# Kernel tuning notes

Measured on AMD Instinct MI355X. Metric: run time of the kernel, lower is better.

The kernel has to match this reference:

```python
import jax, jax.numpy as jnp
import numpy as np

# Model dims
B, S, H, E, I, K = 2, 2048, 1024, 8, 1024, 2
ALPHA, LIMIT = 1.702, 7.0  # gpt_oss activation constants (module defaults)


def setup_inputs() -> dict:
    key = jax.random.key(0)
    ks = jax.random.split(key, 5)
    sc = 0.02
    return {
        "hidden_states": jax.random.normal(ks[0], (B, S, H), jnp.float32),
        "router_weight": jax.random.normal(ks[1], (H, E), jnp.float32) * sc,
        "gate_up_proj": jax.random.normal(ks[2], (E, H, 2 * I), jnp.float32) * sc,
        "gate_up_proj_bias": jnp.zeros((E, 2 * I), jnp.float32),
        "down_proj": jax.random.normal(ks[3], (E, I, H), jnp.float32) * sc,
        "down_proj_bias": jnp.zeros((E, H), jnp.float32),
    }


def reference(hidden_states, router_weight, gate_up_proj, gate_up_proj_bias,
              down_proj, down_proj_bias):
    Bt, St, Ht = hidden_states.shape
    x = hidden_states.reshape(-1, Ht)           # [T, H], T = B*S
    T = x.shape[0]

    # Router: linear -> top-k -> softmax over selected logits (gpt_oss style)
    logits = x @ router_weight                  # [T, E]
    top_vals, top_idx = jax.lax.top_k(logits, K)
    scores = jax.nn.softmax(top_vals, axis=-1)  # [T, K]
    # Sparse combine weights: w[t, e] = score if e selected for t, else 0
    w = jnp.zeros((T, E), x.dtype).at[jnp.arange(T)[:, None], top_idx].set(scores)

    # Fused gate+up projection for every expert (dense equivalent of grouped GEMM;
    # unselected experts get zero combine weight so math matches sparse path)
    gu = jnp.einsum('th,ehf->tef', x, gate_up_proj) + gate_up_proj_bias  # [T, E, 2I]
    gate = gu[..., ::2]                         # interleaved gate (default)
    up = gu[..., 1::2]
    gate = jnp.minimum(gate, LIMIT)
    up = jnp.clip(up, -LIMIT, LIMIT)
    glu = gate * jax.nn.sigmoid(gate * ALPHA)
    act = (up + 1.0) * glu                      # [T, E, I]

    down = jnp.einsum('tei,eih->teh', act, down_proj) + down_proj_bias  # [T, E, H]

    # Weighted combine over experts (all-to-all combine is identity at D=1)
    out = jnp.einsum('te,teh->th', w, down)     # [T, H]
    return out.reshape(Bt, St, Ht)
```

## Files before the change

kernel.cpp:

```cpp
#include <hip/hip_runtime.h>
#include <hip/hip_bf16.h>
#include <cstdint>
#include <cstddef>

constexpr int T_TOK = 4096;
constexpr int H_DIM = 1024;
constexpr int E_NUM = 8;
constexpr int I_DIM = 1024;
constexpr int F2    = 2048;
constexpr float ALPHA = 1.702f;
constexpr float LIMIT = 7.0f;
constexpr int BM = 256;
constexpr int BK = 32;
constexpr int NT = 32;
constexpr int MAXT = 40;

using u16    = unsigned short;
using bf16x8 = __attribute__((ext_vector_type(8))) __bf16;
using s16x8  = __attribute__((ext_vector_type(8))) short;
using f32x4  = __attribute__((ext_vector_type(4))) float;

constexpr size_t WS_W1T  = 0;
constexpr size_t WS_DOWN = 0;
constexpr size_t WS_W2T  = 33554432;
constexpr size_t WS_ACT  = 50331648;
constexpr size_t WS_ETOK = 71303168;
constexpr size_t WS_POS  = 71434240;
constexpr size_t WS_CNT  = 71467008;
constexpr size_t WS_ROWB = 71467040;
constexpr size_t WS_ASGN = 71467072;
constexpr size_t WS_TOPE = 71468096;
constexpr size_t WS_TOPW = 71484480;
constexpr size_t WS_XBF  = 71517248;
constexpr size_t WS_NEED = 79905856;

__device__ __forceinline__ u16 f2bf(float f) {
    union { float f; unsigned u; } v; v.f = f;
    return (u16)((v.u + 0x7FFFu + ((v.u >> 16) & 1u)) >> 16);
}
__device__ __forceinline__ float bf2f(u16 u) {
    union { unsigned u; float f; } v; v.u = (unsigned)u << 16; return v.f;
}

__device__ __forceinline__ s16x8 pack8(float4 a, float4 b) {
    s16x8 r;
    r[0] = (short)f2bf(a.x); r[1] = (short)f2bf(a.y);
    r[2] = (short)f2bf(a.z); r[3] = (short)f2bf(a.w);
    r[4] = (short)f2bf(b.x); r[5] = (short)f2bf(b.y);
    r[6] = (short)f2bf(b.z); r[7] = (short)f2bf(b.w);
    return r;
}

__device__ __forceinline__ void gload16(const void* g, void* l) {
    __builtin_amdgcn_global_load_lds((const __attribute__((address_space(1))) unsigned*)g,
                                     (__attribute__((address_space(3))) unsigned*)l,
                                     16, 0, 0);
}

__device__ __forceinline__ void pipe_sync() {
    __builtin_amdgcn_sched_barrier(0);
    asm volatile("s_waitcnt vmcnt(0) lgkmcnt(0)" ::: "memory");
    __builtin_amdgcn_s_barrier();
    __builtin_amdgcn_sched_barrier(0);
}

__global__ __launch_bounds__(256) void k_xbf(const float* __restrict__ x,
                                             u16* __restrict__ xbf) {
    const size_t i = ((size_t)blockIdx.x * 256 + threadIdx.x) * 8;
    float4 a = *(const float4*)(x + i);
    float4 b = *(const float4*)(x + i + 4);
    *(s16x8*)(xbf + i) = pack8(a, b);
}

__global__ __launch_bounds__(256) void k_transpose_w1(const float* __restrict__ in,
                                                      u16* __restrict__ out) {
    __shared__ float tile[64][65];
    const int e = blockIdx.z, c0 = blockIdx.x * 64, h0 = blockIdx.y * 64;
    const int tid = threadIdx.x;
    const float* src = in + ((size_t)e * H_DIM + h0) * F2 + c0;
#pragma unroll
    for (int i = 0; i < 4; ++i) {
        int r = (tid >> 4) + i * 16, c = (tid & 15) * 4;
        float4 v = *(const float4*)(src + (size_t)r * F2 + c);
        tile[r][c] = v.x; tile[r][c + 1] = v.y; tile[r][c + 2] = v.z; tile[r][c + 3] = v.w;
    }
    __syncthreads();
    const int c = tid >> 2, hseg = (tid & 3) * 16;
    const int g = c & 1;
    const int f = (c0 + c) >> 1;
    s16x8 o0, o1;
#pragma unroll
    for (int j = 0; j < 8; ++j) o0[j] = (short)f2bf(tile[hseg + j][c]);
#pragma unroll
    for (int j = 0; j < 8; ++j) o1[j] = (short)f2bf(tile[hseg + 8 + j][c]);
    const int pan = f >> 6;
    const int brow = g * 64 + (f & 63);
    const int h1 = h0 + hseg;
    const int kt = h1 >> 5;
    const int s0 = (h1 & 31) >> 3;
    const int xr = (brow >> 1) & 3;
    u16* blk = out + (((size_t)(e * 16 + pan) * 32 + kt) << 12);
    *(s16x8*)(blk + brow * 32 + ((s0 ^ xr) << 3))       = o0;
    *(s16x8*)(blk + brow * 32 + (((s0 + 1) ^ xr) << 3)) = o1;
}

__global__ __launch_bounds__(256) void k_transpose_w2(const float* __restrict__ in,
                                                      u16* __restrict__ out) {
    __shared__ float tile[64][65];
    const int e = blockIdx.z, h0 = blockIdx.x * 64, i0 = blockIdx.y * 64;
    const int tid = threadIdx.x;
    const float* src = in + ((size_t)e * I_DIM + i0) * H_DIM + h0;
#pragma unroll
    for (int i = 0; i < 4; ++i) {
        int r = (tid >> 4) + i * 16, c = (tid & 15) * 4;
        float4 v = *(const float4*)(src + (size_t)r * H_DIM + c);
        tile[r][c] = v.x; tile[r][c + 1] = v.y; tile[r][c + 2] = v.z; tile[r][c + 3] = v.w;
    }
    __syncthreads();
    const int c = tid >> 2, iseg = (tid & 3) * 16;
    s16x8 o0, o1;
#pragma unroll
    for (int j = 0; j < 8; ++j) o0[j] = (short)f2bf(tile[iseg + j][c]);
#pragma unroll
    for (int j = 0; j < 8; ++j) o1[j] = (short)f2bf(tile[iseg + 8 + j][c]);
    const int hcol = h0 + c;
    const int pan = hcol >> 7;
    const int brow = hcol & 127;
    const int i1 = i0 + iseg;
    const int kt = i1 >> 5;
    const int s0 = (i1 & 31) >> 3;
    const int xr = (brow >> 1) & 3;
    u16* blk = out + (((size_t)(e * 8 + pan) * 32 + kt) << 12);
    *(s16x8*)(blk + brow * 32 + ((s0 ^ xr) << 3))       = o0;
    *(s16x8*)(blk + brow * 32 + (((s0 + 1) ^ xr) << 3)) = o1;
}

__global__ __launch_bounds__(256) void k_router_top2(const float* __restrict__ x,
                                                     const float* __restrict__ rw,
                                                     int* __restrict__ tope,
                                                     float2* __restrict__ topw) {
    const int wave = threadIdx.x >> 6, lane = threadIdx.x & 63;
    const int t = blockIdx.x * 4 + wave;
    const float* xr = x + (size_t)t * H_DIM;
    float acc[E_NUM];
#pragma unroll
    for (int e = 0; e < E_NUM; ++e) acc[e] = 0.f;
    for (int h = lane; h < H_DIM; h += 64) {
        float xv = xr[h];
        const float* r = rw + h * E_NUM;
#pragma unroll
        for (int e = 0; e < E_NUM; ++e) acc[e] += xv * r[e];
    }
#pragma unroll
    for (int e = 0; e < E_NUM; ++e) {
        float v = acc[e];
#pragma unroll
        for (int o = 32; o > 0; o >>= 1) v += __shfl_down(v, o);
        acc[e] = v;
    }
    if (lane == 0) {
        int e0 = 0; float v0 = acc[0];
#pragma unroll
        for (int e = 1; e < E_NUM; ++e) if (acc[e] > v0) { v0 = acc[e]; e0 = e; }
        int e1 = -1; float v1 = -3.4e38f;
#pragma unroll
        for (int e = 0; e < E_NUM; ++e) if (e != e0 && acc[e] > v1) { v1 = acc[e]; e1 = e; }
        float ew = expf(v1 - v0);
        float inv = 1.f / (1.f + ew);
        tope[t] = e0 | (e1 << 8);
        topw[t] = make_float2(inv, ew * inv);
    }
}

__global__ __launch_bounds__(256) void k_router_scatter(const int* __restrict__ tope,
                                                        int* __restrict__ cnt,
                                                        int* __restrict__ ent_tok,
                                                        int2* __restrict__ pos) {
    __shared__ int lcnt[E_NUM];
    __shared__ int gbase[E_NUM];
    const int tid = threadIdx.x;
    const int t = blockIdx.x * 256 + tid;
    if (tid < E_NUM) lcnt[tid] = 0;
    __syncthreads();
    const int pk = tope[t];
    const int e0 = pk & 0xff, e1 = pk >> 8;
    const int o0 = atomicAdd(&lcnt[e0], 1);
    const int o1 = atomicAdd(&lcnt[e1], 1);
    __syncthreads();
    if (tid < E_NUM) gbase[tid] = atomicAdd(&cnt[tid], lcnt[tid]);
    __syncthreads();
    const int p0 = gbase[e0] + o0;
    const int p1 = gbase[e1] + o1;
    ent_tok[e0 * T_TOK + p0] = t;
    ent_tok[e1 * T_TOK + p1] = t;
    pos[t] = make_int2(p0, p1);
}

__global__ void k_schedule(const int* __restrict__ cnt, int* __restrict__ rowbase,
                           int* __restrict__ assign) {
    if (threadIdx.x == 0) {
        int rb = 0, na = 0;
        for (int e = 0; e < E_NUM; ++e) {
            rowbase[e] = rb;
            int nt = (cnt[e] + BM - 1) >> 8;
            for (int m = 0; m < nt; ++m) assign[na++] = (e << 16) | m;
            rb += cnt[e];
            rb = (rb + 255) & ~255;
        }
        for (; na < MAXT; ++na) assign[na] = -1;
    }
}

__global__ __launch_bounds__(512, 4) void k_gemm1(
    const u16* __restrict__ xbf, const u16* __restrict__ w1t,
    const float* __restrict__ bias, const int* __restrict__ ent_tok,
    const int* __restrict__ cnt, const int* __restrict__ rowbase,
    const int* __restrict__ assign, u16* __restrict__ act) {
    const int a = assign[blockIdx.y];
    if (a < 0) return;
    const int e = a >> 16, mt = a & 0xffff;
    const int pan = blockIdx.x;
    const int j0 = pan * 64;
    const int cs = cnt[e], r0 = mt * BM;
    __shared__ __align__(16) u16 As[2][BM * BK];
    __shared__ __align__(16) u16 Bs[2][128 * BK];
    const int tid = threadIdx.x, lane = tid & 63, wv = tid >> 6;
    const int lr = lane >> 2;
    const int sm = (lane & 3) ^ ((lr >> 1) & 3);
    const u16* asrc[2]; int dofsA[2];
#pragma unroll
    for (int j = 0; j < 2; ++j) {
        const int row = wv * 32 + j * 16 + lr;
        const int aent = r0 + row;
        const int tok = (aent < cs) ? ent_tok[e * T_TOK + aent] : 0;
        asrc[j] = xbf + (size_t)tok * H_DIM + sm * 8;
        dofsA[j] = (wv * 32 + j * 16) * BK;
    }
    const u16* bblk = w1t + ((size_t)(e * 16 + pan) * 32) * 4096 + wv * 512 + lane * 8;
    const int dofsB = wv * 512;
    const int wm = wv >> 1, wn = wv & 1;
    const int lcol = lane & 15, lk = lane >> 4;
    int aoff[4], goff[2], uoff[2];
#pragma unroll
    for (int mi = 0; mi < 4; ++mi) {
        const int r = wm * 64 + mi * 16 + lcol;
        aoff[mi] = r * 64 + ((lk ^ ((r >> 1) & 3)) << 4);
    }
#pragma unroll
    for (int nj = 0; nj < 2; ++nj) {
        const int rg_ = wn * 32 + nj * 16 + lcol;
        const int ru  = 64 + rg_;
        goff[nj] = rg_ * 64 + ((lk ^ ((rg_ >> 1) & 3)) << 4);
        uoff[nj] = ru  * 64 + ((lk ^ ((ru  >> 1) & 3)) << 4);
    }
    f32x4 ag[4][2], au[4][2];
    const f32x4 z = {0.f, 0.f, 0.f, 0.f};
#pragma unroll
    for (int mi = 0; mi < 4; ++mi) { ag[mi][0] = z; ag[mi][1] = z; au[mi][0] = z; au[mi][1] = z; }
#pragma unroll
    for (int j = 0; j < 2; ++j) gload16(asrc[j], &As[0][dofsA[j]]);
    gload16(bblk, &Bs[0][dofsB]);
    pipe_sync();
    int cur = 0;
    for (int t = 0; t < NT; ++t) {
        if (t + 1 < NT) {
            const int kn = (t + 1) * BK;
            u16* Ad = As[cur ^ 1]; u16* Bd = Bs[cur ^ 1];
#pragma unroll
            for (int j = 0; j < 2; ++j) gload16(asrc[j] + kn, Ad + dofsA[j]);
            gload16(bblk + (t + 1) * 4096, Bd + dofsB);
        }
        const char* Ab = (const char*)As[cur];
        const char* Bb = (const char*)Bs[cur];
        bf16x8 af[4];
#pragma unroll
        for (int mi = 0; mi < 4; ++mi) af[mi] = *(const bf16x8*)(Ab + aoff[mi]);
        const bf16x8 g0 = *(const bf16x8*)(Bb + goff[0]);
        const bf16x8 g1 = *(const bf16x8*)(Bb + goff[1]);
        const bf16x8 u0 = *(const bf16x8*)(Bb + uoff[0]);
        const bf16x8 u1 = *(const bf16x8*)(Bb + uoff[1]);
#pragma unroll
        for (int mi = 0; mi < 4; ++mi) {
            ag[mi][0] = __builtin_amdgcn_mfma_f32_16x16x32_bf16(af[mi], g0, ag[mi][0], 0, 0, 0);
            au[mi][0] = __builtin_amdgcn_mfma_f32_16x16x32_bf16(af[mi], u0, au[mi][0], 0, 0, 0);
            ag[mi][1] = __builtin_amdgcn_mfma_f32_16x16x32_bf16(af[mi], g1, ag[mi][1], 0, 0, 0);
            au[mi][1] = __builtin_amdgcn_mfma_f32_16x16x32_bf16(af[mi], u1, au[mi][1], 0, 0, 0);
        }
        pipe_sync();
        cur ^= 1;
    }
    const int rbase = rowbase[e];
#pragma unroll
    for (int mi = 0; mi < 4; ++mi) {
#pragma unroll
        for (int nj = 0; nj < 2; ++nj) {
            const int col = j0 + wn * 32 + nj * 16 + lcol;
            const float bg_ = bias[e * F2 + 2 * col];
            const float bu_ = bias[e * F2 + 2 * col + 1];
            const int kt = col >> 5, slot = (col & 31) >> 3, ke = col & 7;
#pragma unroll
            for (int rg = 0; rg < 4; ++rg) {
                const int r = wm * 64 + mi * 16 + lk * 4 + rg;
                if (r0 + r < cs) {
                    float gv = ag[mi][nj][rg] + bg_;
                    float uv = au[mi][nj][rg] + bu_;
                    gv = fminf(gv, LIMIT);
                    uv = fminf(fmaxf(uv, -LIMIT), LIMIT);
                    const float glu = gv / (1.f + expf(-ALPHA * gv));
                    const int grow = rbase + r0 + r;
                    const int rr = grow & 255;
                    act[((size_t)(grow >> 8) * 32 + kt) * 8192 + rr * 32 +
                        ((slot ^ ((rr >> 1) & 3)) << 3) + ke] = f2bf((uv + 1.f) * glu);
                }
            }
        }
    }
}

__global__ __launch_bounds__(512, 4) void k_gemm2(
    const u16* __restrict__ actb, const u16* __restrict__ w2t,
    const int* __restrict__ cnt, const int* __restrict__ rowbase,
    const int* __restrict__ assign, u16* __restrict__ down) {
    const int a = assign[blockIdx.y];
    if (a < 0) return;
    const int e = a >> 16, mt = a & 0xffff;
    const int pan = blockIdx.x;
    const int n0 = pan * 128;
    const int cs = cnt[e], r0 = mt * BM, rbase = rowbase[e];
    __shared__ __align__(16) u16 As[2][BM * BK];
    __shared__ __align__(16) u16 Bs[2][128 * BK];
    const int tid = threadIdx.x, lane = tid & 63, wv = tid >> 6;
    const u16* ablk = actb + ((size_t)((rbase + r0) >> 8) * 32) * 8192 + wv * 1024 + lane * 8;
    const u16* bblk = w2t + ((size_t)(e * 8 + pan) * 32) * 4096 + wv * 512 + lane * 8;
    const int dofsB = wv * 512;
    const int wm = wv >> 1, wn = wv & 1;
    const int lcol = lane & 15, lk = lane >> 4;
    int aoff[4], boff[4];
#pragma unroll
    for (int mi = 0; mi < 4; ++mi) {
        const int r = wm * 64 + mi * 16 + lcol;
        aoff[mi] = r * 64 + ((lk ^ ((r >> 1) & 3)) << 4);
    }
#pragma unroll
    for (int nj = 0; nj < 4; ++nj) {
        const int b = wn * 64 + nj * 16 + lcol;
        boff[nj] = b * 64 + ((lk ^ ((b >> 1) & 3)) << 4);
    }
    f32x4 acc[4][4];
    const f32x4 z = {0.f, 0.f, 0.f, 0.f};
#pragma unroll
    for (int mi = 0; mi < 4; ++mi)
#pragma unroll
        for (int nj = 0; nj < 4; ++nj) acc[mi][nj] = z;
#pragma unroll
    for (int j = 0; j < 2; ++j) gload16(ablk + j * 512, &As[0][wv * 1024 + j * 512]);
    gload16(bblk, &Bs[0][dofsB]);
    pipe_sync();
    int cur = 0;
    for (int t = 0; t < NT; ++t) {
        if (t + 1 < NT) {
            u16* Ad = As[cur ^ 1]; u16* Bd = Bs[cur ^ 1];
#pragma unroll
            for (int j = 0; j < 2; ++j)
                gload16(ablk + (t + 1) * 8192 + j * 512, Ad + wv * 1024 + j * 512);
            gload16(bblk + (t + 1) * 4096, Bd + dofsB);
        }
        const char* Ab = (const char*)As[cur];
        const char* Bb = (const char*)Bs[cur];
        bf16x8 af[4], bf_[4];
#pragma unroll
        for (int mi = 0; mi < 4; ++mi) af[mi]  = *(const bf16x8*)(Ab + aoff[mi]);
#pragma unroll
        for (int nj = 0; nj < 4; ++nj) bf_[nj] = *(const bf16x8*)(Bb + boff[nj]);
#pragma unroll
        for (int mi = 0; mi < 4; ++mi)
#pragma unroll
            for (int nj = 0; nj < 4; ++nj)
                acc[mi][nj] = __builtin_amdgcn_mfma_f32_16x16x32_bf16(af[mi], bf_[nj], acc[mi][nj], 0, 0, 0);
        pipe_sync();
        cur ^= 1;
    }
#pragma unroll
    for (int mi = 0; mi < 4; ++mi) {
#pragma unroll
        for (int nj = 0; nj < 4; ++nj) {
            const int col = n0 + wn * 64 + nj * 16 + lcol;
#pragma unroll
            for (int rg = 0; rg < 4; ++rg) {
                const int r = wm * 64 + mi * 16 + lk * 4 + rg;
                if (r0 + r < cs)
                    down[(size_t)(rbase + r0 + r) * H_DIM + col] = f2bf(acc[mi][nj][rg]);
            }
        }
    }
}

__global__ __launch_bounds__(256) void k_combine(
    const int* __restrict__ tope, const float2* __restrict__ topw,
    const int2* __restrict__ pos, const int* __restrict__ rowb,
    const float* __restrict__ b2, const u16* __restrict__ down,
    float* __restrict__ out) {
    const int t = blockIdx.x;
    const int c = threadIdx.x * 4;
    const int pk = tope[t];
    const int e0 = pk & 0xff, e1 = pk >> 8;
    const int2 pp = pos[t];
    const float2 w = topw[t];
    const size_t ro0 = (size_t)(rowb[e0] + pp.x) * H_DIM;
    const size_t ro1 = (size_t)(rowb[e1] + pp.y) * H_DIM;
    ushort4 d0 = *(const ushort4*)(down + ro0 + c);
    ushort4 d1 = *(const ushort4*)(down + ro1 + c);
    float4 bb0 = *(const float4*)(b2 + e0 * H_DIM + c);
    float4 bb1 = *(const float4*)(b2 + e1 * H_DIM + c);
    float4 o;
    o.x = w.x * (bf2f(d0.x) + bb0.x) + w.y * (bf2f(d1.x) + bb1.x);
    o.y = w.x * (bf2f(d0.y) + bb0.y) + w.y * (bf2f(d1.y) + bb1.y);
    o.z = w.x * (bf2f(d0.z) + bb0.z) + w.y * (bf2f(d1.z) + bb1.z);
    o.w = w.x * (bf2f(d0.w) + bb0.w) + w.y * (bf2f(d1.w) + bb1.w);
    *(float4*)(out + (size_t)t * H_DIM + c) = o;
}

extern "C" void kernel_launch(void* const* d_in, const int* in_sizes, int n_in,
                              void* d_out, int out_size, void* d_ws, size_t ws_size,
                              hipStream_t stream) {
    const float* x   = (const float*)d_in[0];
    const float* rw  = (const float*)d_in[1];
    const float* w1  = (const float*)d_in[2];
    const float* b1  = (const float*)d_in[3];
    const float* w2  = (const float*)d_in[4];
    const float* b2  = (const float*)d_in[5];
    float* out = (float*)d_out;
    char* ws = (char*)d_ws;

    if (ws_size < WS_NEED) return;

    u16*    W1T  = (u16*)(ws + WS_W1T);
    u16*    DOWN = (u16*)(ws + WS_DOWN);
    u16*    W2T  = (u16*)(ws + WS_W2T);
    u16*    ACT  = (u16*)(ws + WS_ACT);
    int*    ETOK = (int*)(ws + WS_ETOK);
    int2*   POS  = (int2*)(ws + WS_POS);
    int*    CNT  = (int*)(ws + WS_CNT);
    int*    ROWB = (int*)(ws + WS_ROWB);
    int*    ASGN = (int*)(ws + WS_ASGN);
    int*    TOPE = (int*)(ws + WS_TOPE);
    float2* TOPW = (float2*)(ws + WS_TOPW);
    u16*    XBF  = (u16*)(ws + WS_XBF);

    hipMemsetAsync(CNT, 0, E_NUM * sizeof(int), stream);

    k_xbf<<<T_TOK * H_DIM / 2048, 256, 0, stream>>>(x, XBF);
    k_transpose_w1<<<dim3(32, 16, 8), 256, 0, stream>>>(w1, W1T);
    k_transpose_w2<<<dim3(16, 16, 8), 256, 0, stream>>>(w2, W2T);
    k_router_top2<<<T_TOK / 4, 256, 0, stream>>>(x, rw, TOPE, TOPW);
    k_router_scatter<<<T_TOK / 256, 256, 0, stream>>>(TOPE, CNT, ETOK, POS);
    k_schedule<<<1, 64, 0, stream>>>(CNT, ROWB, ASGN);
    k_gemm1<<<dim3(16, MAXT), 512, 0, stream>>>(XBF, W1T, b1, ETOK, CNT, ROWB, ASGN, ACT);
    k_gemm2<<<dim3(8, MAXT), 512, 0, stream>>>(ACT, W2T, CNT, ROWB, ASGN, DOWN);
    k_combine<<<T_TOK, 256, 0, stream>>>(TOPE, TOPW, POS, ROWB, b2, DOWN, out);
}
```

Baseline: 163.4 us.

## Triple-buffer LDS stages in both expert GEMMs with partial vmcnt waits

Both grouped GEMM kernels move from a double-buffered LDS pipeline to a three-stage ring. Each iteration issues the loads two K-steps ahead, and a partial `s_waitcnt vmcnt` waits only for the current stage's data instead of draining every outstanding load. The aim is to hide more global-load latency behind the MFMA work. In exchange, LDS use per block grows by half, which can cut how many blocks fit on a CU.

```diff
diff --git a/kernel.cpp b/kernel.cpp
--- a/kernel.cpp
+++ b/kernel.cpp
@@ -57,12 +57,9 @@
                                      16, 0, 0);
 }
 
-__device__ __forceinline__ void pipe_sync() {
-    __builtin_amdgcn_sched_barrier(0);
-    asm volatile("s_waitcnt vmcnt(0) lgkmcnt(0)" ::: "memory");
-    __builtin_amdgcn_s_barrier();
-    __builtin_amdgcn_sched_barrier(0);
-}
+#define SB0() __builtin_amdgcn_sched_barrier(0)
+#define BARC() do { SB0(); __builtin_amdgcn_s_barrier(); SB0(); } while (0)
+#define WVM(n) do { SB0(); asm volatile("s_waitcnt vmcnt(" #n ")" ::: "memory"); } while (0)
 
 __global__ __launch_bounds__(256) void k_xbf(const float* __restrict__ x,
                                              u16* __restrict__ xbf) {
@@ -222,8 +219,8 @@
     const int pan = blockIdx.x;
     const int j0 = pan * 64;
     const int cs = cnt[e], r0 = mt * BM;
-    __shared__ __align__(16) u16 As[2][BM * BK];
-    __shared__ __align__(16) u16 Bs[2][128 * BK];
+    __shared__ __align__(16) u16 As[3][BM * BK];
+    __shared__ __align__(16) u16 Bs[3][128 * BK];
     const int tid = threadIdx.x, lane = tid & 63, wv = tid >> 6;
     const int lr = lane >> 2;
     const int sm = (lane & 3) ^ ((lr >> 1) & 3);
@@ -257,21 +254,25 @@
     const f32x4 z = {0.f, 0.f, 0.f, 0.f};
 #pragma unroll
     for (int mi = 0; mi < 4; ++mi) { ag[mi][0] = z; ag[mi][1] = z; au[mi][0] = z; au[mi][1] = z; }
-#pragma unroll
-    for (int j = 0; j < 2; ++j) gload16(asrc[j], &As[0][dofsA[j]]);
-    gload16(bblk, &Bs[0][dofsB]);
-    pipe_sync();
-    int cur = 0;
+
+#define G1_STAGE(kt, Ad, Bd) do {                                           \
+        const int kn_ = (kt) * BK;                                          \
+        _Pragma("unroll") for (int j = 0; j < 2; ++j)                       \
+            gload16(asrc[j] + kn_, (Ad) + dofsA[j]);                        \
+        gload16(bblk + (size_t)(kt) * 4096, (Bd) + dofsB);                  \
+    } while (0)
+
+    G1_STAGE(0, As[0], Bs[0]);
+    G1_STAGE(1, As[1], Bs[1]);
+    u16 *Ar = As[0], *An = As[1], *Af = As[2];
+    u16 *Br = Bs[0], *Bn = Bs[1], *Bf = Bs[2];
     for (int t = 0; t < NT; ++t) {
-        if (t + 1 < NT) {
-            const int kn = (t + 1) * BK;
-            u16* Ad = As[cur ^ 1]; u16* Bd = Bs[cur ^ 1];
-#pragma unroll
-            for (int j = 0; j < 2; ++j) gload16(asrc[j] + kn, Ad + dofsA[j]);
-            gload16(bblk + (t + 1) * 4096, Bd + dofsB);
-        }
-        const char* Ab = (const char*)As[cur];
-        const char* Bb = (const char*)Bs[cur];
+        if (t + 2 < NT) { G1_STAGE(t + 2, Af, Bf); WVM(6); }
+        else if (t + 1 < NT) { WVM(3); }
+        else { WVM(0); }
+        BARC();
+        const char* Ab = (const char*)Ar;
+        const char* Bb = (const char*)Br;
         bf16x8 af[4];
 #pragma unroll
         for (int mi = 0; mi < 4; ++mi) af[mi] = *(const bf16x8*)(Ab + aoff[mi]);
@@ -286,9 +287,11 @@
             ag[mi][1] = __builtin_amdgcn_mfma_f32_16x16x32_bf16(af[mi], g1, ag[mi][1], 0, 0, 0);
             au[mi][1] = __builtin_amdgcn_mfma_f32_16x16x32_bf16(af[mi], u1, au[mi][1], 0, 0, 0);
         }
-        pipe_sync();
-        cur ^= 1;
-    }
+        BARC();
+        u16* tA = Ar; Ar = An; An = Af; Af = tA;
+        u16* tB = Br; Br = Bn; Bn = Bf; Bf = tB;
+    }
+#undef G1_STAGE
     const int rbase = rowbase[e];
 #pragma unroll
     for (int mi = 0; mi < 4; ++mi) {
@@ -327,8 +330,8 @@
     const int pan = blockIdx.x;
     const int n0 = pan * 128;
     const int cs = cnt[e], r0 = mt * BM, rbase = rowbase[e];
-    __shared__ __align__(16) u16 As[2][BM * BK];
-    __shared__ __align__(16) u16 Bs[2][128 * BK];
+    __shared__ __align__(16) u16 As[3][BM * BK];
+    __shared__ __align__(16) u16 Bs[3][128 * BK];
     const int tid = threadIdx.x, lane = tid & 63, wv = tid >> 6;
     const u16* ablk = actb + ((size_t)((rbase + r0) >> 8) * 32) * 8192 + wv * 1024 + lane * 8;
     const u16* bblk = w2t + ((size_t)(e * 8 + pan) * 32) * 4096 + wv * 512 + lane * 8;
@@ -352,21 +355,25 @@
     for (int mi = 0; mi < 4; ++mi)
 #pragma unroll
         for (int nj = 0; nj < 4; ++nj) acc[mi][nj] = z;
-#pragma unroll
-    for (int j = 0; j < 2; ++j) gload16(ablk + j * 512, &As[0][wv * 1024 + j * 512]);
-    gload16(bblk, &Bs[0][dofsB]);
-    pipe_sync();
-    int cur = 0;
+
+#define G2_STAGE(kt, Ad, Bd) do {                                           \
+        _Pragma("unroll") for (int j = 0; j < 2; ++j)                       \
+            gload16(ablk + (size_t)(kt) * 8192 + j * 512,                   \
+                    (Ad) + wv * 1024 + j * 512);                            \
+        gload16(bblk + (size_t)(kt) * 4096, (Bd) + dofsB);                  \
+    } while (0)
+
+    G2_STAGE(0, As[0], Bs[0]);
+    G2_STAGE(1, As[1], Bs[1]);
+    u16 *Ar = As[0], *An = As[1], *Af = As[2];
+    u16 *Br = Bs[0], *Bn = Bs[1], *Bf = Bs[2];
     for (int t = 0; t < NT; ++t) {
-        if (t + 1 < NT) {
-            u16* Ad = As[cur ^ 1]; u16* Bd = Bs[cur ^ 1];
-#pragma unroll
-            for (int j = 0; j < 2; ++j)
-                gload16(ablk + (t + 1) * 8192 + j * 512, Ad + wv * 1024 + j * 512);
-            gload16(bblk + (t + 1) * 4096, Bd + dofsB);
-        }
-        const char* Ab = (const char*)As[cur];
-        const char* Bb = (const char*)Bs[cur];
+        if (t + 2 < NT) { G2_STAGE(t + 2, Af, Bf); WVM(6); }
+        else if (t + 1 < NT) { WVM(3); }
+        else { WVM(0); }
+        BARC();
+        const char* Ab = (const char*)Ar;
+        const char* Bb = (const char*)Br;
         bf16x8 af[4], bf_[4];
 #pragma unroll
         for (int mi = 0; mi < 4; ++mi) af[mi]  = *(const bf16x8*)(Ab + aoff[mi]);
@@ -377,9 +384,11 @@
 #pragma unroll
             for (int nj = 0; nj < 4; ++nj)
                 acc[mi][nj] = __builtin_amdgcn_mfma_f32_16x16x32_bf16(af[mi], bf_[nj], acc[mi][nj], 0, 0, 0);
-        pipe_sync();
-        cur ^= 1;
-    }
+        BARC();
+        u16* tA = Ar; Ar = An; An = Af; Af = tA;
+        u16* tB = Br; Br = Bn; Bn = Bf; Bf = tB;
+    }
+#undef G2_STAGE
 #pragma unroll
     for (int mi = 0; mi < 4; ++mi) {
 #pragma unroll
```

After: 165.3 us. Within noise of the previous version (+1.2%).

## Fuse weighted combine into down-projection GEMM epilogue via atomic adds

Applied to the files above, without the earlier changes.

Removes the separate combine kernel and the bf16 intermediate down buffer. The down GEMM epilogue now looks up each row's token and routing weight, adds the bias, scales, and atomically adds the result into the fp32 output, which is zeroed by a memset first. This saves a full write and read of the down intermediate and one launch. In exchange it adds the memset plus scattered fp32 atomics with only 16-column contiguity per lane group, and the summation order becomes nondeterministic. The schedule kernel is also rewritten to stage counts and assignments through shared memory.

```diff
diff --git a/kernel.cpp b/kernel.cpp
--- a/kernel.cpp
+++ b/kernel.cpp
@@ -21,25 +21,21 @@
 using f32x4  = __attribute__((ext_vector_type(4))) float;
 
 constexpr size_t WS_W1T  = 0;
-constexpr size_t WS_DOWN = 0;
 constexpr size_t WS_W2T  = 33554432;
 constexpr size_t WS_ACT  = 50331648;
 constexpr size_t WS_ETOK = 71303168;
-constexpr size_t WS_POS  = 71434240;
-constexpr size_t WS_CNT  = 71467008;
-constexpr size_t WS_ROWB = 71467040;
-constexpr size_t WS_ASGN = 71467072;
-constexpr size_t WS_TOPE = 71468096;
-constexpr size_t WS_TOPW = 71484480;
-constexpr size_t WS_XBF  = 71517248;
-constexpr size_t WS_NEED = 79905856;
+constexpr size_t WS_EW   = 71434240;
+constexpr size_t WS_CNT  = 71565312;
+constexpr size_t WS_ROWB = 71565344;
+constexpr size_t WS_ASGN = 71565376;
+constexpr size_t WS_TOPE = 71566400;
+constexpr size_t WS_TOPW = 71582784;
+constexpr size_t WS_XBF  = 71615552;
+constexpr size_t WS_NEED = 80004160;
 
 __device__ __forceinline__ u16 f2bf(float f) {
     union { float f; unsigned u; } v; v.f = f;
     return (u16)((v.u + 0x7FFFu + ((v.u >> 16) & 1u)) >> 16);
-}
-__device__ __forceinline__ float bf2f(u16 u) {
-    union { unsigned u; float f; } v; v.u = (unsigned)u << 16; return v.f;
 }
 
 __device__ __forceinline__ s16x8 pack8(float4 a, float4 b) {
@@ -173,9 +169,10 @@
 }
 
 __global__ __launch_bounds__(256) void k_router_scatter(const int* __restrict__ tope,
+                                                        const float2* __restrict__ topw,
                                                         int* __restrict__ cnt,
                                                         int* __restrict__ ent_tok,
-                                                        int2* __restrict__ pos) {
+                                                        float* __restrict__ ent_w) {
     __shared__ int lcnt[E_NUM];
     __shared__ int gbase[E_NUM];
     const int tid = threadIdx.x;
@@ -183,6 +180,7 @@
     if (tid < E_NUM) lcnt[tid] = 0;
     __syncthreads();
     const int pk = tope[t];
+    const float2 w = topw[t];
     const int e0 = pk & 0xff, e1 = pk >> 8;
     const int o0 = atomicAdd(&lcnt[e0], 1);
     const int o1 = atomicAdd(&lcnt[e1], 1);
@@ -191,24 +189,30 @@
     __syncthreads();
     const int p0 = gbase[e0] + o0;
     const int p1 = gbase[e1] + o1;
-    ent_tok[e0 * T_TOK + p0] = t;
-    ent_tok[e1 * T_TOK + p1] = t;
-    pos[t] = make_int2(p0, p1);
+    ent_tok[e0 * T_TOK + p0] = t; ent_w[e0 * T_TOK + p0] = w.x;
+    ent_tok[e1 * T_TOK + p1] = t; ent_w[e1 * T_TOK + p1] = w.y;
 }
 
 __global__ void k_schedule(const int* __restrict__ cnt, int* __restrict__ rowbase,
                            int* __restrict__ assign) {
-    if (threadIdx.x == 0) {
+    __shared__ int sc[E_NUM], srb[E_NUM], sasg[MAXT];
+    const int tid = threadIdx.x;
+    if (tid < E_NUM) sc[tid] = cnt[tid];
+    __syncthreads();
+    if (tid == 0) {
         int rb = 0, na = 0;
         for (int e = 0; e < E_NUM; ++e) {
-            rowbase[e] = rb;
-            int nt = (cnt[e] + BM - 1) >> 8;
-            for (int m = 0; m < nt; ++m) assign[na++] = (e << 16) | m;
-            rb += cnt[e];
+            srb[e] = rb;
+            const int nt = (sc[e] + 255) >> 8;
+            for (int m = 0; m < nt; ++m) sasg[na++] = (e << 16) | m;
+            rb += sc[e];
             rb = (rb + 255) & ~255;
         }
-        for (; na < MAXT; ++na) assign[na] = -1;
-    }
+        for (; na < MAXT; ++na) sasg[na] = -1;
+    }
+    __syncthreads();
+    if (tid < E_NUM) rowbase[tid] = srb[tid];
+    if (tid < MAXT) assign[tid] = sasg[tid];
 }
 
 __global__ __launch_bounds__(512, 4) void k_gemm1(
@@ -268,7 +272,7 @@
             u16* Ad = As[cur ^ 1]; u16* Bd = Bs[cur ^ 1];
 #pragma unroll
             for (int j = 0; j < 2; ++j) gload16(asrc[j] + kn, Ad + dofsA[j]);
-            gload16(bblk + (t + 1) * 4096, Bd + dofsB);
+            gload16(bblk + (size_t)(t + 1) * 4096, Bd + dofsB);
         }
         const char* Ab = (const char*)As[cur];
         const char* Bb = (const char*)Bs[cur];
@@ -319,8 +323,10 @@
 
 __global__ __launch_bounds__(512, 4) void k_gemm2(
     const u16* __restrict__ actb, const u16* __restrict__ w2t,
-    const int* __restrict__ cnt, const int* __restrict__ rowbase,
-    const int* __restrict__ assign, u16* __restrict__ down) {
+    const float* __restrict__ b2, const int* __restrict__ ent_tok,
+    const float* __restrict__ ent_w, const int* __restrict__ cnt,
+    const int* __restrict__ rowbase, const int* __restrict__ assign,
+    float* __restrict__ out) {
     const int a = assign[blockIdx.y];
     if (a < 0) return;
     const int e = a >> 16, mt = a & 0xffff;
@@ -362,8 +368,8 @@
             u16* Ad = As[cur ^ 1]; u16* Bd = Bs[cur ^ 1];
 #pragma unroll
             for (int j = 0; j < 2; ++j)
-                gload16(ablk + (t + 1) * 8192 + j * 512, Ad + wv * 1024 + j * 512);
-            gload16(bblk + (t + 1) * 4096, Bd + dofsB);
+                gload16(ablk + (size_t)(t + 1) * 8192 + j * 512, Ad + wv * 1024 + j * 512);
+            gload16(bblk + (size_t)(t + 1) * 4096, Bd + dofsB);
         }
         const char* Ab = (const char*)As[cur];
         const char* Bb = (const char*)Bs[cur];
@@ -383,41 +389,21 @@
 #pragma unroll
     for (int mi = 0; mi < 4; ++mi) {
 #pragma unroll
-        for (int nj = 0; nj < 4; ++nj) {
-            const int col = n0 + wn * 64 + nj * 16 + lcol;
-#pragma unroll
-            for (int rg = 0; rg < 4; ++rg) {
-                const int r = wm * 64 + mi * 16 + lk * 4 + rg;
-                if (r0 + r < cs)
-                    down[(size_t)(rbase + r0 + r) * H_DIM + col] = f2bf(acc[mi][nj][rg]);
+        for (int rg = 0; rg < 4; ++rg) {
+            const int r = wm * 64 + mi * 16 + lk * 4 + rg;
+            const int ent = r0 + r;
+            if (ent < cs) {
+                const int tok = ent_tok[e * T_TOK + ent];
+                const float w = ent_w[e * T_TOK + ent];
+#pragma unroll
+                for (int nj = 0; nj < 4; ++nj) {
+                    const int col = n0 + wn * 64 + nj * 16 + lcol;
+                    atomicAdd(&out[(size_t)tok * H_DIM + col],
+                              w * (acc[mi][nj][rg] + b2[e * H_DIM + col]));
+                }
             }
         }
     }
-}
-
-__global__ __launch_bounds__(256) void k_combine(
-    const int* __restrict__ tope, const float2* __restrict__ topw,
-    const int2* __restrict__ pos, const int* __restrict__ rowb,
-    const float* __restrict__ b2, const u16* __restrict__ down,
-    float* __restrict__ out) {
-    const int t = blockIdx.x;
-    const int c = threadIdx.x * 4;
-    const int pk = tope[t];
-    const int e0 = pk & 0xff, e1 = pk >> 8;
-    const int2 pp = pos[t];
-    const float2 w = topw[t];
-    const size_t ro0 = (size_t)(rowb[e0] + pp.x) * H_DIM;
-    const size_t ro1 = (size_t)(rowb[e1] + pp.y) * H_DIM;
-    ushort4 d0 = *(const ushort4*)(down + ro0 + c);
-    ushort4 d1 = *(const ushort4*)(down + ro1 + c);
-    float4 bb0 = *(const float4*)(b2 + e0 * H_DIM + c);
-    float4 bb1 = *(const float4*)(b2 + e1 * H_DIM + c);
-    float4 o;
-    o.x = w.x * (bf2f(d0.x) + bb0.x) + w.y * (bf2f(d1.x) + bb1.x);
-    o.y = w.x * (bf2f(d0.y) + bb0.y) + w.y * (bf2f(d1.y) + bb1.y);
-    o.z = w.x * (bf2f(d0.z) + bb0.z) + w.y * (bf2f(d1.z) + bb1.z);
-    o.w = w.x * (bf2f(d0.w) + bb0.w) + w.y * (bf2f(d1.w) + bb1.w);
-    *(float4*)(out + (size_t)t * H_DIM + c) = o;
 }
 
 extern "C" void kernel_launch(void* const* d_in, const int* in_sizes, int n_in,
@@ -435,11 +421,10 @@
     if (ws_size < WS_NEED) return;
 
     u16*    W1T  = (u16*)(ws + WS_W1T);
-    u16*    DOWN = (u16*)(ws + WS_DOWN);
     u16*    W2T  = (u16*)(ws + WS_W2T);
     u16*    ACT  = (u16*)(ws + WS_ACT);
     int*    ETOK = (int*)(ws + WS_ETOK);
-    int2*   POS  = (int2*)(ws + WS_POS);
+    float*  EW   = (float*)(ws + WS_EW);
     int*    CNT  = (int*)(ws + WS_CNT);
     int*    ROWB = (int*)(ws + WS_ROWB);
     int*    ASGN = (int*)(ws + WS_ASGN);
@@ -448,14 +433,14 @@
     u16*    XBF  = (u16*)(ws + WS_XBF);
 
     hipMemsetAsync(CNT, 0, E_NUM * sizeof(int), stream);
+    hipMemsetAsync(out, 0, (size_t)T_TOK * H_DIM * sizeof(float), stream);
 
     k_xbf<<<T_TOK * H_DIM / 2048, 256, 0, stream>>>(x, XBF);
     k_transpose_w1<<<dim3(32, 16, 8), 256, 0, stream>>>(w1, W1T);
     k_transpose_w2<<<dim3(16, 16, 8), 256, 0, stream>>>(w2, W2T);
     k_router_top2<<<T_TOK / 4, 256, 0, stream>>>(x, rw, TOPE, TOPW);
-    k_router_scatter<<<T_TOK / 256, 256, 0, stream>>>(TOPE, CNT, ETOK, POS);
+    k_router_scatter<<<T_TOK / 256, 256, 0, stream>>>(TOPE, TOPW, CNT, ETOK, EW);
     k_schedule<<<1, 64, 0, stream>>>(CNT, ROWB, ASGN);
     k_gemm1<<<dim3(16, MAXT), 512, 0, stream>>>(XBF, W1T, b1, ETOK, CNT, ROWB, ASGN, ACT);
-    k_gemm2<<<dim3(8, MAXT), 512, 0, stream>>>(ACT, W2T, CNT, ROWB, ASGN, DOWN);
-    k_combine<<<T_TOK, 256, 0, stream>>>(TOPE, TOPW, POS, ROWB, b2, DOWN, out);
-}
+    k_gemm2<<<dim3(8, MAXT), 512, 0, stream>>>(ACT, W2T, b2, ETOK, EW, CNT, ROWB, ASGN, out);
+}
```

Result: slower. 184.2 us (+12.7%).
